# Performance work log

Hardware: AMD Instinct MI355X
Metric: run time of the kernel (lower is better)

## Reference

```python
import jax, jax.numpy as jnp
import numpy as np

EPS = 1e-5

def layernorm(x, w, b):
    m = jnp.mean(x, axis=-1, keepdims=True)
    v = jnp.var(x, axis=-1, keepdims=True)
    return (x - m) * jax.lax.rsqrt(v + EPS) * w + b

def setup_inputs() -> dict:
    key = jax.random.key(0)
    ks = jax.random.split(key, 20)
    B, N, D, H, C = 4, 2048, 512, 8, 3
    HID = int(D * 4.0 * (2.0 / 3.0))  # SwiGLU hidden = 1365
    g = lambda k, shape, s: (jax.random.normal(k, shape, jnp.float32) * s)
    return {
        "x": g(ks[0], (B, N, D), 1.0),
        "coords": jax.random.uniform(ks[1], (B, N, C), jnp.float32),
        "ln1_w": jnp.ones((D,), jnp.float32),
        "ln1_b": jnp.zeros((D,), jnp.float32),
        "ln2_w": jnp.ones((D,), jnp.float32),
        "ln2_b": jnp.zeros((D,), jnp.float32),
        "Wqkv": g(ks[2], (D, 3 * D), D ** -0.5),
        "bqkv": jnp.zeros((3 * D,), jnp.float32),
        "Wo": g(ks[3], (D, D), D ** -0.5),
        "bo": jnp.zeros((D,), jnp.float32),
        "Wc": g(ks[4], (C, H), 0.1),
        "bc": jnp.zeros((H,), jnp.float32),
        "W1": g(ks[5], (D, HID), D ** -0.5),
        "b1": jnp.zeros((HID,), jnp.float32),
        "W2": g(ks[6], (D, HID), D ** -0.5),
        "b2": jnp.zeros((HID,), jnp.float32),
        "W3": g(ks[7], (HID, D), HID ** -0.5),
        "b3": jnp.zeros((D,), jnp.float32),
    }

def reference(x, coords, ln1_w, ln1_b, ln2_w, ln2_b, Wqkv, bqkv, Wo, bo,
              Wc, bc, W1, b1, W2, b2, W3, b3):
    B, N, D = x.shape
    H = bc.shape[0]
    dh = D // H
    # --- coord-aware patch attention (pre-norm) ---
    h = layernorm(x, ln1_w, ln1_b)
    qkv = h @ Wqkv + bqkv                                # [B,N,3D]
    q, k, v = jnp.split(qkv, 3, axis=-1)
    to_heads = lambda t: t.reshape(B, N, H, dh).transpose(0, 2, 1, 3)  # [B,H,N,dh]
    q, k, v = to_heads(q), to_heads(k), to_heads(v)
    scores = jnp.einsum("bhnd,bhmd->bhnm", q, k) / np.sqrt(dh)
    rel = coords[:, :, None, :] - coords[:, None, :, :]  # [B,N,N,C]
    bias = jnp.einsum("bnmc,ch->bhnm", rel, Wc) + bc[None, :, None, None]
    attn = jax.nn.softmax(scores + bias, axis=-1)
    o = jnp.einsum("bhnm,bhmd->bhnd", attn, v)
    o = o.transpose(0, 2, 1, 3).reshape(B, N, D)
    x = x + (o @ Wo + bo)                                # residual 1
    # --- SwiGLU FFN (pre-norm) ---
    h2 = layernorm(x, ln2_w, ln2_b)
    ff = jax.nn.silu(h2 @ W1 + b1) * (h2 @ W2 + b2)
    x = x + (ff @ W3 + b3)                               # residual 2
    return x
```

## Files before the change

### kernel.cpp

```cpp
#include <hip/hip_runtime.h>
#include <hip/hip_bf16.h>
#include <math.h>

#define B_   4
#define N_   2048
#define D_   512
#define H_   8
#define DH_  64
#define C_   3
#define HID_ 1365
#define HIDP 1408
#define ROWS_ (B_*N_)
#define TD_  (3*D_)

typedef __attribute__((ext_vector_type(8))) short short8;
typedef __attribute__((ext_vector_type(4))) float floatx4;
typedef __attribute__((ext_vector_type(2))) unsigned uint2v;

#define MFMA16(a,b,c) __builtin_amdgcn_mfma_f32_16x16x32_bf16(a,b,c,0,0,0)

typedef __attribute__((address_space(3))) unsigned lds_u32;
typedef __attribute__((address_space(1))) unsigned glb_u32;

__device__ __forceinline__ short sh(float v){
  union { __hip_bfloat16 b; short s; } u;
  u.b = __float2bfloat16(v);
  return u.s;
}

__device__ __forceinline__ unsigned pk2(float a, float b){
  union { short s[2]; unsigned u; } z;
  z.s[0] = sh(a); z.s[1] = sh(b);
  return z.u;
}

__device__ __forceinline__ int swz(int col, int row){
  return (col & ~63) | (col & 7) | ((((col >> 3) & 7) ^ (row & 7)) << 3);
}

__device__ __forceinline__ int xcdswz(int bid, int nwg){
  return (bid & 7) * (nwg >> 3) + (bid >> 3);
}

template<int ROWS, int PITCH, int WAVES = 4>
__device__ __forceinline__ void stageG(short* __restrict__ lds,
    const short* __restrict__ g, int ldg, int t){
  const int LPR = PITCH/8;
  const int RPI = 64/LPR;
  const int PW  = (ROWS/RPI)/WAVES;
  int lane = t & 63, w = t >> 6;
  #pragma unroll
  for (int i = 0; i < PW; ++i){
    int r0  = (w*PW + i)*RPI;
    int row = r0 + lane/LPR;
    const short* ga = g + (size_t)row*ldg + (lane % LPR)*8;
    short* la = lds + r0*PITCH;
    __builtin_amdgcn_global_load_lds((const glb_u32*)ga, (lds_u32*)la, 16, 0, 0);
  }
}

__device__ __forceinline__ short8 fragS(const short* __restrict__ lds, int pitch,
    int mbase, int lane, int kk){
  int row  = mbase + (lane & 15);
  int seg  = (kk >> 3) + (lane >> 4);
  int phys = seg ^ (row & 7);
  return *(const short8*)(lds + row*pitch + phys*8);
}

__global__ __launch_bounds__(256) void convT_all(
    const float* __restrict__ Wqkv, const float* __restrict__ Wo,
    const float* __restrict__ W1, const float* __restrict__ W2,
    const float* __restrict__ W3,
    short* __restrict__ Wtqkv, short* __restrict__ Wto,
    short* __restrict__ Wt1, short* __restrict__ Wt2, short* __restrict__ Wt3,
    const float* __restrict__ coords, const float* __restrict__ Wc,
    float* __restrict__ tv,
    const float* __restrict__ x, const float* __restrict__ ln1_w,
    const float* __restrict__ ln1_b, short* __restrict__ h){
  int id = blockIdx.x;
  int t = threadIdx.x;
  if (id >= 3392){
    int row = id - 3392;
    size_t base = (size_t)row * D_;
    float2 u = *(const float2*)&x[base + 2*t];
    float s  = u.x + u.y;
    float s2 = u.x*u.x + u.y*u.y;
    #pragma unroll
    for (int off = 32; off >= 1; off >>= 1){
      s  += __shfl_xor(s,  off, 64);
      s2 += __shfl_xor(s2, off, 64);
    }
    __shared__ float red[8];
    int lane = t & 63, wv = t >> 6;
    if (lane == 0){ red[wv] = s; red[4+wv] = s2; }
    __syncthreads();
    float sum  = red[0]+red[1]+red[2]+red[3];
    float sum2 = red[4]+red[5]+red[6]+red[7];
    float mean = sum * (1.0f/D_);
    float var  = sum2 * (1.0f/D_) - mean*mean;
    float inv  = rsqrtf(fmaxf(var, 0.f) + 1e-5f);
    float2 wv2 = *(const float2*)&ln1_w[2*t];
    float2 bv2 = *(const float2*)&ln1_b[2*t];
    *(unsigned*)(h + base + swz(2*t, row)) =
        pk2((u.x-mean)*inv*wv2.x + bv2.x, (u.y-mean)*inv*wv2.y + bv2.y);
    return;
  }
  if (id >= 3136){
    int idx = (id - 3136)*256 + t;
    int n = idx & (N_-1);
    int hh = (idx >> 11) & (H_-1);
    int b = idx >> 14;
    float s = 0.f;
    #pragma unroll
    for (int cc = 0; cc < C_; ++cc)
      s += coords[((size_t)(b*N_+n))*C_ + cc] * Wc[cc*H_ + hh];
    tv[idx] = s * 1.44269504f;
    return;
  }
  __shared__ float tile[32][33];
  const float* in; short* out; int K, NN, Kp, nx;
  if (id < 768)      { in=Wqkv; out=Wtqkv; K=512;  NN=1536; Kp=512;  nx=48; }
  else if (id < 1024){ in=Wo;   out=Wto;   K=512;  NN=512;  Kp=512;  nx=16; id-=768; }
  else if (id < 1728){ in=W1;   out=Wt1;   K=512;  NN=HID_; Kp=512;  nx=44; id-=1024; }
  else if (id < 2432){ in=W2;   out=Wt2;   K=512;  NN=HID_; Kp=512;  nx=44; id-=1728; }
  else               { in=W3;   out=Wt3;   K=HID_; NN=512;  Kp=HIDP; nx=16; id-=2432; }
  int nt0 = (id % nx)*32, kt0 = (id / nx)*32;
  int r = t >> 5, cc = t & 31;
  #pragma unroll
  for (int i=0;i<4;++i){
    int k = kt0 + i*8 + r, n = nt0 + cc;
    tile[i*8+r][cc] = (k<K && n<NN) ? in[(size_t)k*NN + n] : 0.f;
  }
  __syncthreads();
  #pragma unroll
  for (int i=0;i<4;++i){
    int n = nt0 + i*8 + r, k = kt0 + cc;
    out[(size_t)n*Kp + swz(k, n)] = sh(tile[cc][i*8+r]);
  }
}

__global__ __launch_bounds__(256) void ln_kernel(const float* __restrict__ x,
        const float* __restrict__ w, const float* __restrict__ b,
        short* __restrict__ out){
  int row = blockIdx.x;
  size_t base = (size_t)row * D_;
  int t = threadIdx.x;
  float2 u = *(const float2*)&x[base + 2*t];
  float s  = u.x + u.y;
  float s2 = u.x*u.x + u.y*u.y;
  #pragma unroll
  for (int off = 32; off >= 1; off >>= 1){
    s  += __shfl_xor(s,  off, 64);
    s2 += __shfl_xor(s2, off, 64);
  }
  __shared__ float red[8];
  int lane = t & 63, wv = t >> 6;
  if (lane == 0){ red[wv] = s; red[4+wv] = s2; }
  __syncthreads();
  float sum  = red[0]+red[1]+red[2]+red[3];
  float sum2 = red[4]+red[5]+red[6]+red[7];
  float mean = sum * (1.0f/D_);
  float var  = sum2 * (1.0f/D_) - mean*mean;
  float inv  = rsqrtf(fmaxf(var, 0.f) + 1e-5f);
  float2 wv2 = *(const float2*)&w[2*t];
  float2 bv2 = *(const float2*)&b[2*t];
  *(unsigned*)(out + base + swz(2*t, row)) =
      pk2((u.x-mean)*inv*wv2.x + bv2.x, (u.y-mean)*inv*wv2.y + bv2.y);
}

__global__ __launch_bounds__(256) void qkv_gemm(
    const short* __restrict__ A, const short* __restrict__ Bt,
    const float* __restrict__ bias,
    short* __restrict__ qb, short* __restrict__ kb, short* __restrict__ vbt){
  __shared__ short As[2][128*64];
  __shared__ short Bs[2][128*64];
  int t = threadIdx.x;
  int lane = t & 63, w = t >> 6;
  int wr = (w >> 1) * 64, wc = (w & 1) * 64;
  int wg = xcdswz(blockIdx.x, 768);
  int colblk = wg % 12, rowblk = wg / 12;
  int col0 = colblk * 128, row0 = rowblk * 128;
  bool vblk = (colblk >= 8);
  floatx4 acc[4][4];
  #pragma unroll
  for (int mt=0;mt<4;++mt)
    #pragma unroll
    for (int nt=0;nt<4;++nt) acc[mt][nt] = (floatx4){0.f,0.f,0.f,0.f};
  stageG<128,64>(As[0], A  + (size_t)row0*D_, D_, t);
  stageG<128,64>(Bs[0], Bt + (size_t)col0*D_, D_, t);
  for (int ti = 0; ti < 8; ++ti){
    int cur = ti & 1;
    __syncthreads();
    if (ti + 1 < 8){
      stageG<128,64>(As[cur^1], A  + (size_t)row0*D_ + (ti+1)*64, D_, t);
      stageG<128,64>(Bs[cur^1], Bt + (size_t)col0*D_ + (ti+1)*64, D_, t);
    }
    #pragma unroll
    for (int kk = 0; kk < 64; kk += 32){
      short8 af[4], bf[4];
      #pragma unroll
      for (int mt=0;mt<4;++mt) af[mt] = fragS(As[cur], 64, wr+mt*16, lane, kk);
      #pragma unroll
      for (int nt=0;nt<4;++nt) bf[nt] = fragS(Bs[cur], 64, wc+nt*16, lane, kk);
      if (vblk){
        #pragma unroll
        for (int mt=0;mt<4;++mt)
          #pragma unroll
          for (int nt=0;nt<4;++nt)
            acc[mt][nt] = MFMA16(af[mt], bf[nt], acc[mt][nt]);
      } else {
        #pragma unroll
        for (int mt=0;mt<4;++mt)
          #pragma unroll
          for (int nt=0;nt<4;++nt)
            acc[mt][nt] = MFMA16(bf[nt], af[mt], acc[mt][nt]);
      }
    }
  }
  int quad = lane >> 4, c = lane & 15;
  if (vblk){
    #pragma unroll
    for (int mt=0;mt<4;++mt){
      int rb0 = row0 + wr + mt*16 + quad*4;
      int bidx = rb0 >> 11, n0 = rb0 & (N_-1);
      #pragma unroll
      for (int nt=0;nt<4;++nt){
        int col = col0 + wc + nt*16 + c;
        int d = col & (D_-1), hh = d >> 6, hd = d & 63;
        float bc = bias[col];
        uint2v pv;
        pv.x = pk2(acc[mt][nt][0]+bc, acc[mt][nt][1]+bc);
        pv.y = pk2(acc[mt][nt][2]+bc, acc[mt][nt][3]+bc);
        *(uint2v*)(vbt + (((size_t)(bidx*H_ + hh))*DH_ + hd)*N_ + swz(n0, hd)) = pv;
      }
    }
  } else {
    #pragma unroll
    for (int mt=0;mt<4;++mt){
      int row = row0 + wr + mt*16 + c;
      int bidx = row >> 11, n = row & (N_-1);
      #pragma unroll
      for (int nt=0;nt<4;++nt){
        int d0 = col0 + wc + nt*16 + quad*4;
        floatx4 b4 = *(const floatx4*)&bias[d0];
        int which = d0 >> 9, dd = d0 & (D_-1), hh = dd >> 6, hd0 = dd & 63;
        short* dst = which ? kb : qb;
        uint2v pv;
        pv.x = pk2(acc[mt][nt][0]+b4[0], acc[mt][nt][1]+b4[1]);
        pv.y = pk2(acc[mt][nt][2]+b4[2], acc[mt][nt][3]+b4[3]);
        *(uint2v*)(dst + (((size_t)(bidx*H_ + hh))*N_ + n)*DH_ + swz(hd0, n)) = pv;
      }
    }
  }
}

__global__ __launch_bounds__(256) void gemm64(
    const short* __restrict__ A, int lda,
    const short* __restrict__ Bt, int Ktot,
    const float* __restrict__ bias,
    const float* __restrict__ resid, float* __restrict__ outF){
  __shared__ short As[2][128*64];
  __shared__ short Bs[2][64*64];
  int t = threadIdx.x, lane = t & 63, w = t >> 6;
  int wr = w * 32;
  int wg = xcdswz(blockIdx.x, 512);
  int col0 = (wg & 7) * 64, row0 = (wg >> 3) * 128;
  floatx4 acc[2][4];
  #pragma unroll
  for (int mt=0;mt<2;++mt)
    #pragma unroll
    for (int nt=0;nt<4;++nt) acc[mt][nt] = (floatx4){0.f,0.f,0.f,0.f};
  stageG<128,64>(As[0], A  + (size_t)row0*lda, lda, t);
  stageG<64,64> (Bs[0], Bt + (size_t)col0*Ktot, Ktot, t);
  const int NT = Ktot >> 6;
  for (int ti = 0; ti < NT; ++ti){
    int cur = ti & 1;
    __syncthreads();
    if (ti + 1 < NT){
      stageG<128,64>(As[cur^1], A  + (size_t)row0*lda + (ti+1)*64, lda, t);
      stageG<64,64> (Bs[cur^1], Bt + (size_t)col0*Ktot + (ti+1)*64, Ktot, t);
    }
    #pragma unroll
    for (int kk = 0; kk < 64; kk += 32){
      short8 af[2], bf[4];
      #pragma unroll
      for (int mt=0;mt<2;++mt) af[mt] = fragS(As[cur], 64, wr+mt*16, lane, kk);
      #pragma unroll
      for (int nt=0;nt<4;++nt) bf[nt] = fragS(Bs[cur], 64, nt*16, lane, kk);
      #pragma unroll
      for (int mt=0;mt<2;++mt)
        #pragma unroll
        for (int nt=0;nt<4;++nt)
          acc[mt][nt] = MFMA16(bf[nt], af[mt], acc[mt][nt]);
    }
  }
  int quad = lane >> 4, c = lane & 15;
  #pragma unroll
  for (int mt=0;mt<2;++mt){
    int row = row0 + wr + mt*16 + c;
    #pragma unroll
    for (int nt=0;nt<4;++nt){
      int c0 = col0 + nt*16 + quad*4;
      size_t idx = (size_t)row*D_ + c0;
      float4 rv = *(const float4*)&resid[idx];
      floatx4 b4 = *(const floatx4*)&bias[c0];
      float4 ov;
      ov.x = acc[mt][nt][0] + b4[0] + rv.x;
      ov.y = acc[mt][nt][1] + b4[1] + rv.y;
      ov.z = acc[mt][nt][2] + b4[2] + rv.z;
      ov.w = acc[mt][nt][3] + b4[3] + rv.w;
      *(float4*)&outF[idx] = ov;
    }
  }
}

__global__ __launch_bounds__(256) void gate_gemm(
    const short* __restrict__ A,
    const short* __restrict__ Bt1, const short* __restrict__ Bt2,
    const float* __restrict__ b1, const float* __restrict__ b2,
    short* __restrict__ ff){
  __shared__ short As[128*64];
  __shared__ short B1s[64*64];
  __shared__ short B2s[64*64];
  int t = threadIdx.x, lane = t & 63, w = t >> 6;
  int wr = (w >> 1) * 64, wc = (w & 1) * 32;
  int wg = xcdswz(blockIdx.x, 1408);
  int col0 = (wg % 22) * 64, row0 = (wg / 22) * 128;
  floatx4 a1[4][2], a2[4][2];
  #pragma unroll
  for (int mt=0;mt<4;++mt)
    #pragma unroll
    for (int nt=0;nt<2;++nt){
      a1[mt][nt] = (floatx4){0.f,0.f,0.f,0.f};
      a2[mt][nt] = (floatx4){0.f,0.f,0.f,0.f};
    }
  for (int k0 = 0; k0 < D_; k0 += 64){
    __syncthreads();
    stageG<128,64>(As, A + (size_t)row0*D_ + k0, D_, t);
    stageG<64,64>(B1s, Bt1 + (size_t)col0*D_ + k0, D_, t);
    stageG<64,64>(B2s, Bt2 + (size_t)col0*D_ + k0, D_, t);
    __syncthreads();
    #pragma unroll
    for (int kk = 0; kk < 64; kk += 32){
      short8 af[4], f1[2], f2[2];
      #pragma unroll
      for (int mt=0;mt<4;++mt) af[mt] = fragS(As, 64, wr+mt*16, lane, kk);
      #pragma unroll
      for (int nt=0;nt<2;++nt){
        f1[nt] = fragS(B1s, 64, wc+nt*16, lane, kk);
        f2[nt] = fragS(B2s, 64, wc+nt*16, lane, kk);
      }
      #pragma unroll
      for (int mt=0;mt<4;++mt)
        #pragma unroll
        for (int nt=0;nt<2;++nt){
          a1[mt][nt] = MFMA16(f1[nt], af[mt], a1[mt][nt]);
          a2[mt][nt] = MFMA16(f2[nt], af[mt], a2[mt][nt]);
        }
    }
  }
  int quad = lane >> 4, c = lane & 15;
  #pragma unroll
  for (int mt=0;mt<4;++mt){
    int row = row0 + wr + mt*16 + c;
    size_t rbase = (size_t)row * HIDP;
    #pragma unroll
    for (int nt=0;nt<2;++nt){
      int c0 = col0 + wc + nt*16 + quad*4;
      float v[4];
      #pragma unroll
      for (int r=0;r<4;++r){
        int col = c0 + r;
        float g1 = a1[mt][nt][r] + (col < HID_ ? b1[col] : 0.f);
        float g2 = a2[mt][nt][r] + (col < HID_ ? b2[col] : 0.f);
        float sig = 1.f / (1.f + __expf(-g1));
        v[r] = g1*sig*g2;
      }
      uint2v pv;
      pv.x = pk2(v[0], v[1]);
      pv.y = pk2(v[2], v[3]);
      *(uint2v*)(ff + rbase + swz(c0, row)) = pv;
    }
  }
}

#define EXP2SC 0.18033688011112042f

#define ZERO_S(S) { \
  S[0][0] = (floatx4){0.f,0.f,0.f,0.f}; S[0][1] = (floatx4){0.f,0.f,0.f,0.f}; \
  S[1][0] = (floatx4){0.f,0.f,0.f,0.f}; S[1][1] = (floatx4){0.f,0.f,0.f,0.f}; }

#define QKT(S, kb) { \
  _Pragma("unroll") \
  for (int kh=0;kh<2;++kh){ \
    short8 kf0 = fragS(Kc, 64, (kb)*32,      lane, kh*32); \
    short8 kf1 = fragS(Kc, 64, (kb)*32 + 16, lane, kh*32); \
    _Pragma("unroll") \
    for (int mt=0;mt<2;++mt){ \
      S[0][mt] = MFMA16(kf0, qf[mt][kh], S[0][mt]); \
      S[1][mt] = MFMA16(kf1, qf[mt][kh], S[1][mt]); \
    } \
  } }

#define SOFTPV(S, kb) { \
  floatx4 t0 = *(const floatx4*)&tsc[(kb)*32 + quad*4]; \
  floatx4 t1 = *(const floatx4*)&tsc[(kb)*32 + 16 + quad*4]; \
  short8 pbf[2]; \
  _Pragma("unroll") \
  for (int mt=0;mt<2;++mt){ \
    float p0[4], p1[4]; \
    _Pragma("unroll") \
    for (int r=0;r<4;++r){ \
      p0[r] = __builtin_amdgcn_exp2f(fmaf(S[0][mt][r], EXP2SC, -t0[r])); \
      p1[r] = __builtin_amdgcn_exp2f(fmaf(S[1][mt][r], EXP2SC, -t1[r])); \
    } \
    l_i[mt] += (p0[0]+p0[1]) + (p0[2]+p0[3]) + (p1[0]+p1[1]) + (p1[2]+p1[3]); \
    unsigned X0 = pk2(p0[0], p0[1]), X1 = pk2(p0[2], p0[3]); \
    unsigned Y0 = pk2(p1[0], p1[1]), Y1 = pk2(p1[2], p1[3]); \
    auto u0 = __builtin_amdgcn_permlane32_swap(X0, Y0, false, false); \
    auto v0 = __builtin_amdgcn_permlane16_swap(u0[0], u0[1], false, false); \
    auto u1 = __builtin_amdgcn_permlane32_swap(X1, Y1, false, false); \
    auto v1 = __builtin_amdgcn_permlane16_swap(u1[0], u1[1], false, false); \
    union { short8 s; unsigned uu[4]; } pb; \
    pb.uu[0] = v0[0]; pb.uu[1] = v1[0]; pb.uu[2] = v0[1]; pb.uu[3] = v1[1]; \
    pbf[mt] = pb.s; \
  } \
  _Pragma("unroll") \
  for (int nt=0;nt<4;++nt){ \
    short8 vf = fragS(Vc, 128, nt*16, lane, (kb)*32); \
    _Pragma("unroll") \
    for (int mt=0;mt<2;++mt) \
      O[mt][nt] = MFMA16(vf, pbf[mt], O[mt][nt]); \
  } }

__global__ __launch_bounds__(256) void attn_mfma(
    const short* __restrict__ qb, const short* __restrict__ kbuf,
    const short* __restrict__ vbt, const float* __restrict__ tv,
    short* __restrict__ o){
  __shared__ short Ks2[2][128*64];
  __shared__ short Vt2[2][64*128];
  __shared__ __align__(16) float tsAll[2048];
  int wg = xcdswz(blockIdx.x, 512);
  int bh = wg >> 4, qt = wg & 15;
  int b = bh >> 3, h = bh & 7;
  int t = threadIdx.x, lane = t & 63, w = t >> 6;
  int quad = lane >> 4, c = lane & 15;
  const short* Kbase = kbuf + (size_t)bh*N_*DH_;
  const short* Vbase = vbt  + (size_t)bh*DH_*N_;

  #pragma unroll
  for (int i = 0; i < 2; ++i)
    *(floatx4*)&tsAll[t*8 + i*4] = *(const floatx4*)&tv[(size_t)bh*N_ + t*8 + i*4];
  stageG<128,64>(Ks2[1], qb + ((size_t)bh*N_ + qt*128)*DH_, DH_, t);
  stageG<128,64>(Ks2[0], Kbase, DH_, t);
  stageG<64,128>(Vt2[0], Vbase, N_, t);
  __syncthreads();
  short8 qf[2][2];
  #pragma unroll
  for (int mt=0;mt<2;++mt)
    #pragma unroll
    for (int kh=0;kh<2;++kh)
      qf[mt][kh] = fragS(Ks2[1], 64, w*32 + mt*16, lane, kh*32);
  floatx4 O[2][4];
  float l_i[2] = {0.f, 0.f};
  #pragma unroll
  for (int mt=0;mt<2;++mt)
    #pragma unroll
    for (int nt=0;nt<4;++nt) O[mt][nt] = (floatx4){0.f,0.f,0.f,0.f};
  __syncthreads();

  for (int kt = 0; kt < N_/128; ++kt){
    int cur = kt & 1;
    if (kt + 1 < N_/128){
      stageG<128,64>(Ks2[cur^1], Kbase + (size_t)(kt+1)*128*DH_, DH_, t);
      stageG<64,128>(Vt2[cur^1], Vbase + (kt+1)*128, N_, t);
    }
    const short* Kc  = Ks2[cur];
    const short* Vc  = Vt2[cur];
    const float* tsc = tsAll + kt*128;
    floatx4 Sa[2][2], Sb[2][2];
    ZERO_S(Sa); QKT(Sa, 0);
    ZERO_S(Sb); QKT(Sb, 1);
    SOFTPV(Sa, 0);
    ZERO_S(Sa); QKT(Sa, 2);
    SOFTPV(Sb, 1);
    ZERO_S(Sb); QKT(Sb, 3);
    SOFTPV(Sa, 2);
    SOFTPV(Sb, 3);
    __syncthreads();
  }
  #pragma unroll
  for (int mt=0;mt<2;++mt){
    float l = l_i[mt];
    l += __shfl_xor(l, 16, 64);
    l += __shfl_xor(l, 32, 64);
    float invl = 1.f / l;
    int qrow = qt*128 + w*32 + mt*16 + c;
    size_t rb = ((size_t)b*N_ + qrow)*(size_t)D_;
    #pragma unroll
    for (int nt=0;nt<4;++nt){
      int d0 = h*DH_ + nt*16 + quad*4;
      uint2v pv;
      pv.x = pk2(O[mt][nt][0]*invl, O[mt][nt][1]*invl);
      pv.y = pk2(O[mt][nt][2]*invl, O[mt][nt][3]*invl);
      *(uint2v*)(o + rb + swz(d0, qrow)) = pv;
    }
  }
}

extern "C" void kernel_launch(void* const* d_in, const int* in_sizes, int n_in,
                              void* d_out, int out_size, void* d_ws, size_t ws_size,
                              hipStream_t stream){
  const float* x      = (const float*)d_in[0];
  const float* coords = (const float*)d_in[1];
  const float* ln1_w  = (const float*)d_in[2];
  const float* ln1_b  = (const float*)d_in[3];
  const float* ln2_w  = (const float*)d_in[4];
  const float* ln2_b  = (const float*)d_in[5];
  const float* Wqkv   = (const float*)d_in[6];
  const float* bqkv   = (const float*)d_in[7];
  const float* Wo     = (const float*)d_in[8];
  const float* bo     = (const float*)d_in[9];
  const float* Wc     = (const float*)d_in[10];
  const float* W1     = (const float*)d_in[12];
  const float* b1     = (const float*)d_in[13];
  const float* W2     = (const float*)d_in[14];
  const float* b2     = (const float*)d_in[15];
  const float* W3     = (const float*)d_in[16];
  const float* b3     = (const float*)d_in[17];

  char* ws = (char*)d_ws;
  short* Wtqkv = (short*)(ws);
  short* Wto   = (short*)(ws + 1572864);
  short* Wt1   = (short*)(ws + 2097152);
  short* Wt2   = (short*)(ws + 3538944);
  short* Wt3   = (short*)(ws + 4980736);
  float* tv    = (float*)(ws + 6422528);
  short* h     = (short*)(ws + 6684672);
  short* qb    = (short*)(ws + 15073280);
  short* kb    = (short*)(ws + 23461888);
  short* vbt   = (short*)(ws + 31850496);
  short* o     = h;
  short* h2    = h;
  short* ff    = qb;
  float* x1    = (float*)d_out;

  convT_all<<<dim3(11584), dim3(256), 0, stream>>>(Wqkv, Wo, W1, W2, W3,
      Wtqkv, Wto, Wt1, Wt2, Wt3, coords, Wc, tv, x, ln1_w, ln1_b, h);
  qkv_gemm<<<dim3(768), dim3(256), 0, stream>>>(h, Wtqkv, bqkv, qb, kb, vbt);
  attn_mfma<<<dim3(512), dim3(256), 0, stream>>>(qb, kb, vbt, tv, o);
  gemm64<<<dim3(512), dim3(256), 0, stream>>>(o, 512, Wto, 512, bo, x, x1);
  ln_kernel<<<dim3(ROWS_), dim3(256), 0, stream>>>(x1, ln2_w, ln2_b, h2);
  gate_gemm<<<dim3(1408), dim3(256), 0, stream>>>(h2, Wt1, Wt2, b1, b2, ff);
  gemm64<<<dim3(512), dim3(256), 0, stream>>>(ff, HIDP, Wt3, HIDP, b3, x1, x1);
}
```

Baseline: 277.2 us.

## Compute softmax row sums via MFMA with ones, hoist bias loads, add setprio

Replaces the per-lane VALU accumulation of softmax denominators and the final cross-lane shuffles with an extra MFMA that multiplies the bf16 probability fragment by a ones vector. This moves reduction work onto the matrix unit. The per-tile bias-term LDS loads are hoisted into registers at the start of each key tile, and s_setprio raises wave priority around MFMA blocks to improve interleaving across waves. The row sum now comes from bf16-rounded probabilities, so it is consistent with the values used in PV, but register pressure rises from the treg array.

After: 273.6 us. About the same (-1.3%).

```diff
diff --git a/kernel.cpp b/kernel.cpp
--- a/kernel.cpp
+++ b/kernel.cpp
@@ -395,26 +395,25 @@
   for (int kh=0;kh<2;++kh){ \
     short8 kf0 = fragS(Kc, 64, (kb)*32,      lane, kh*32); \
     short8 kf1 = fragS(Kc, 64, (kb)*32 + 16, lane, kh*32); \
+    __builtin_amdgcn_s_setprio(1); \
     _Pragma("unroll") \
     for (int mt=0;mt<2;++mt){ \
       S[0][mt] = MFMA16(kf0, qf[mt][kh], S[0][mt]); \
       S[1][mt] = MFMA16(kf1, qf[mt][kh], S[1][mt]); \
     } \
+    __builtin_amdgcn_s_setprio(0); \
   } }
 
 #define SOFTPV(S, kb) { \
-  floatx4 t0 = *(const floatx4*)&tsc[(kb)*32 + quad*4]; \
-  floatx4 t1 = *(const floatx4*)&tsc[(kb)*32 + 16 + quad*4]; \
   short8 pbf[2]; \
   _Pragma("unroll") \
   for (int mt=0;mt<2;++mt){ \
     float p0[4], p1[4]; \
     _Pragma("unroll") \
     for (int r=0;r<4;++r){ \
-      p0[r] = __builtin_amdgcn_exp2f(fmaf(S[0][mt][r], EXP2SC, -t0[r])); \
-      p1[r] = __builtin_amdgcn_exp2f(fmaf(S[1][mt][r], EXP2SC, -t1[r])); \
+      p0[r] = __builtin_amdgcn_exp2f(fmaf(S[0][mt][r], EXP2SC, -treg[(kb)*2][r])); \
+      p1[r] = __builtin_amdgcn_exp2f(fmaf(S[1][mt][r], EXP2SC, -treg[(kb)*2+1][r])); \
     } \
-    l_i[mt] += (p0[0]+p0[1]) + (p0[2]+p0[3]) + (p1[0]+p1[1]) + (p1[2]+p1[3]); \
     unsigned X0 = pk2(p0[0], p0[1]), X1 = pk2(p0[2], p0[3]); \
     unsigned Y0 = pk2(p1[0], p1[1]), Y1 = pk2(p1[2], p1[3]); \
     auto u0 = __builtin_amdgcn_permlane32_swap(X0, Y0, false, false); \
@@ -425,13 +424,18 @@
     pb.uu[0] = v0[0]; pb.uu[1] = v1[0]; pb.uu[2] = v0[1]; pb.uu[3] = v1[1]; \
     pbf[mt] = pb.s; \
   } \
+  __builtin_amdgcn_s_setprio(1); \
   _Pragma("unroll") \
   for (int nt=0;nt<4;++nt){ \
     short8 vf = fragS(Vc, 128, nt*16, lane, (kb)*32); \
     _Pragma("unroll") \
     for (int mt=0;mt<2;++mt) \
       O[mt][nt] = MFMA16(vf, pbf[mt], O[mt][nt]); \
-  } }
+  } \
+  Lacc[0] = MFMA16(ones8, pbf[0], Lacc[0]); \
+  Lacc[1] = MFMA16(ones8, pbf[1], Lacc[1]); \
+  __builtin_amdgcn_s_setprio(0); \
+  }
 
 __global__ __launch_bounds__(256) void attn_mfma(
     const short* __restrict__ qb, const short* __restrict__ kbuf,
@@ -447,6 +451,8 @@
   int quad = lane >> 4, c = lane & 15;
   const short* Kbase = kbuf + (size_t)bh*N_*DH_;
   const short* Vbase = vbt  + (size_t)bh*DH_*N_;
+  const short ONEB = (short)0x3F80;
+  short8 ones8 = {ONEB,ONEB,ONEB,ONEB,ONEB,ONEB,ONEB,ONEB};
 
   #pragma unroll
   for (int i = 0; i < 2; ++i)
@@ -462,7 +468,9 @@
     for (int kh=0;kh<2;++kh)
       qf[mt][kh] = fragS(Ks2[1], 64, w*32 + mt*16, lane, kh*32);
   floatx4 O[2][4];
-  float l_i[2] = {0.f, 0.f};
+  floatx4 Lacc[2];
+  Lacc[0] = (floatx4){0.f,0.f,0.f,0.f};
+  Lacc[1] = (floatx4){0.f,0.f,0.f,0.f};
   #pragma unroll
   for (int mt=0;mt<2;++mt)
     #pragma unroll
@@ -478,6 +486,10 @@
     const short* Kc  = Ks2[cur];
     const short* Vc  = Vt2[cur];
     const float* tsc = tsAll + kt*128;
+    floatx4 treg[8];
+    #pragma unroll
+    for (int i = 0; i < 8; ++i)
+      treg[i] = *(const floatx4*)&tsc[i*16 + quad*4];
     floatx4 Sa[2][2], Sb[2][2];
     ZERO_S(Sa); QKT(Sa, 0);
     ZERO_S(Sb); QKT(Sb, 1);
@@ -491,10 +503,7 @@
   }
   #pragma unroll
   for (int mt=0;mt<2;++mt){
-    float l = l_i[mt];
-    l += __shfl_xor(l, 16, 64);
-    l += __shfl_xor(l, 32, 64);
-    float invl = 1.f / l;
+    float invl = 1.f / Lacc[mt][0];
     int qrow = qt*128 + w*32 + mt*16 + c;
     size_t rb = ((size_t)b*N_ + qrow)*(size_t)D_;
     #pragma unroll
```
